# Kernel tuning notes

Hardware: AMD Instinct MI355X
Metric: run time of the kernel (lower is better)

## Reference

```python
import jax, jax.numpy as jnp
import numpy as np

BATCH_SIZE = 4096
DIM = 128
TEMPERATURE = 0.5
EPS = 1e-8


def setup_inputs() -> dict:
    key = jax.random.key(0)
    k1, k2 = jax.random.split(key)
    z_i = jax.random.normal(k1, (BATCH_SIZE, DIM), dtype=jnp.float32)
    z_j = jax.random.normal(k2, (BATCH_SIZE, DIM), dtype=jnp.float32)
    return {"z_i": z_i, "z_j": z_j}


def reference(z_i, z_j):
    B = z_i.shape[0]
    N = 2 * B
    z = jnp.concatenate([z_i, z_j], axis=0)  # [N, D]
    # cosine similarity = matmul of L2-normalized rows (avoids the NxNxD broadcast)
    zn = z / jnp.maximum(jnp.linalg.norm(z, axis=1, keepdims=True), EPS)
    sim = (zn @ zn.T) / TEMPERATURE  # [N, N]
    idx = jnp.arange(N)
    # positive pair: row i pairs with row (i+B) mod N (covers both diag offsets +B and -B)
    pos = sim[idx, (idx + B) % N]  # [N]
    # CE over logits [pos, negatives]; the logit set per row is the full sim row
    # minus the self-similarity (diagonal). Mask diagonal with a large negative.
    neg_inf = jnp.asarray(-1e9, sim.dtype)
    sim_masked = jnp.where(idx[:, None] == idx[None, :], neg_inf, sim)
    lse = jax.nn.logsumexp(sim_masked, axis=1)  # [N]
    # CrossEntropyLoss(reduction='sum') with label 0 (the positive), divided by N
    loss = jnp.sum(lse - pos) / N
    return loss
```

## Files before the change

### kernel.cpp

```cpp
#include <hip/hip_runtime.h>
#include <cstdint>


#define BROWS 4096
#define NROWS 8192
#define ROWB  256
#define CSPL  24
#define CT32  256
#define BRT   256
#define TILEB 8192

typedef __attribute__((ext_vector_type(8))) __bf16    bf16x8;
typedef __attribute__((ext_vector_type(4))) float     f32x4;
typedef __attribute__((ext_vector_type(4))) uint32_t  u32x4;

#define K1F 2.8853900817779268f
#define LN2F 0.69314718055994531f
#define BC8(x) __builtin_bit_cast(bf16x8, x)

__device__ __forceinline__ uint16_t f2bf(float f) {
    uint32_t u = __builtin_bit_cast(uint32_t, f);
    u = (u + 0x7FFFu + ((u >> 16) & 1u)) >> 16;
    return (uint16_t)u;
}
__device__ __forceinline__ float bf2f(uint16_t b) {
    return __builtin_bit_cast(float, ((uint32_t)b) << 16);
}
__device__ __forceinline__ void gload_lds16(const void* g, void* l) {
    __builtin_amdgcn_global_load_lds(
        (const __attribute__((address_space(1))) void*)g,
        (__attribute__((address_space(3))) void*)l, 16, 0, 0);
}

__global__ __launch_bounds__(256) void k_normalize(
    const float* __restrict__ zi, const float* __restrict__ zj,
    uint16_t* __restrict__ znA, uint16_t* __restrict__ znB,
    float* __restrict__ out)
{
    if (blockIdx.x == 0 && threadIdx.x == 0) out[0] = 0.f;

    int tid  = threadIdx.x;
    int lane = tid & 63;
    int wid  = tid >> 6;
    int li   = lane & 7;
    int row  = blockIdx.x * 32 + wid * 8 + (lane >> 3);

    const float* src = (row < BROWS) ? (zi + (size_t)row * 128)
                                     : (zj + (size_t)(row - BROWS) * 128);
    float4 v[4];
    const float4* s4 = (const float4*)(src + li * 16);
#pragma unroll
    for (int c = 0; c < 4; ++c) v[c] = s4[c];

    float ss = 0.f;
#pragma unroll
    for (int c = 0; c < 4; ++c)
        ss += v[c].x*v[c].x + v[c].y*v[c].y + v[c].z*v[c].z + v[c].w*v[c].w;
#pragma unroll
    for (int off = 1; off < 8; off <<= 1) ss += __shfl_xor(ss, off);

    float scale = 1.0f / fmaxf(sqrtf(ss), 1e-8f);

    float e[16];
#pragma unroll
    for (int c = 0; c < 4; ++c) {
        e[c*4+0] = v[c].x * scale; e[c*4+1] = v[c].y * scale;
        e[c*4+2] = v[c].z * scale; e[c*4+3] = v[c].w * scale;
    }
    uint32_t wB[8], wA[8];
#pragma unroll
    for (int q = 0; q < 8; ++q) {
        wB[q] = (uint32_t)f2bf(e[2*q])       | ((uint32_t)f2bf(e[2*q+1])       << 16);
        wA[q] = (uint32_t)f2bf(e[2*q] * K1F) | ((uint32_t)f2bf(e[2*q+1] * K1F) << 16);
    }
    uint4* dB = (uint4*)((char*)znB + (size_t)row * ROWB + li * 32);
    dB[0] = make_uint4(wB[0], wB[1], wB[2], wB[3]);
    dB[1] = make_uint4(wB[4], wB[5], wB[6], wB[7]);
    uint4* dA = (uint4*)((char*)znA + (size_t)row * ROWB + li * 32);
    dA[0] = make_uint4(wA[0], wA[1], wA[2], wA[3]);
    dA[1] = make_uint4(wA[4], wA[5], wA[6], wA[7]);
}

__global__ __launch_bounds__(256)
__attribute__((amdgpu_waves_per_eu(3, 3)))
void k_simlse(
    const uint16_t* __restrict__ znA, const uint16_t* __restrict__ znB,
    float* __restrict__ partial)
{
    __shared__ __align__(16) char lds[3][TILEB];

    const char* zA = (const char*)znA;
    const char* zB = (const char*)znB;
    int tid  = threadIdx.x;
    int lane = tid & 63;
    int wid  = tid >> 6;
    int lo16 = lane & 15;
    int hi4  = lane >> 4;
    int rowBase = blockIdx.x * BRT + wid * 64;

    u32x4 a[4][4];
#pragma unroll
    for (int rt = 0; rt < 4; ++rt) {
        const char* ap = zA + (size_t)(rowBase + rt * 16 + lo16) * ROWB + hi4 * 16;
#pragma unroll
        for (int kf = 0; kf < 4; ++kf)
            a[rt][kf] = *(const u32x4*)(ap + kf * 64);
    }

    float rs[4][4];
#pragma unroll
    for (int rt = 0; rt < 4; ++rt)
#pragma unroll
        for (int r = 0; r < 4; ++r) rs[rt][r] = 0.f;

    int t0 = (CT32 * blockIdx.y) / CSPL;
    int t1 = (CT32 * (blockIdx.y + 1)) / CSPL;
    int nt = t1 - t0;

    const char* gsrc = zB + (size_t)t0 * TILEB
                     + ((tid * 16) ^ (((tid >> 4) & 7) << 4));
    int xorv = (lo16 & 7) << 4;

#define STAGE(sel, t) do {                                                     \
        const char* g_ = gsrc + (size_t)(t) * TILEB;                           \
        gload_lds16(g_,        &lds[sel][wid * 1024]);                         \
        gload_lds16(g_ + 4096, &lds[sel][4096 + wid * 1024]);                  \
    } while (0)

#define COMPUTE(sel) do {                                                        \
        _Pragma("unroll")                                                        \
        for (int ct = 0; ct < 2; ++ct) {                                         \
            const char* lb_ = &lds[sel][ct * 4096 + lo16 * 256];                 \
            u32x4 bf[4];                                                         \
            _Pragma("unroll")                                                    \
            for (int kf = 0; kf < 4; ++kf)                                       \
                bf[kf] = *(const u32x4*)(lb_ + ((hi4 * 16 + kf * 64) ^ xorv));   \
            f32x4 ac0 = {0.f,0.f,0.f,0.f}, ac1 = {0.f,0.f,0.f,0.f};              \
            f32x4 ac2 = {0.f,0.f,0.f,0.f}, ac3 = {0.f,0.f,0.f,0.f};              \
            _Pragma("unroll")                                                    \
            for (int kf = 0; kf < 4; ++kf) {                                     \
                bf16x8 bk_ = BC8(bf[kf]);                                        \
                ac0 = __builtin_amdgcn_mfma_f32_16x16x32_bf16(BC8(a[0][kf]), bk_, ac0, 0, 0, 0); \
                ac1 = __builtin_amdgcn_mfma_f32_16x16x32_bf16(BC8(a[1][kf]), bk_, ac1, 0, 0, 0); \
                ac2 = __builtin_amdgcn_mfma_f32_16x16x32_bf16(BC8(a[2][kf]), bk_, ac2, 0, 0, 0); \
                ac3 = __builtin_amdgcn_mfma_f32_16x16x32_bf16(BC8(a[3][kf]), bk_, ac3, 0, 0, 0); \
            }                                                                    \
            _Pragma("unroll")                                                    \
            for (int r = 0; r < 4; ++r) {                                        \
                rs[0][r] += __builtin_amdgcn_exp2f(ac0[r]);                      \
                rs[1][r] += __builtin_amdgcn_exp2f(ac1[r]);                      \
                rs[2][r] += __builtin_amdgcn_exp2f(ac2[r]);                      \
                rs[3][r] += __builtin_amdgcn_exp2f(ac3[r]);                      \
            }                                                                    \
        }                                                                        \
    } while (0)

    STAGE(0, 0);
    STAGE(1, 1);

    int t = 0;
    for (; t < nt - 1; ++t) {
        asm volatile("s_waitcnt vmcnt(2)" ::: "memory");
        __builtin_amdgcn_s_barrier();
        __builtin_amdgcn_sched_barrier(0);
        COMPUTE(t % 3);
        if (t + 2 < nt) STAGE((t + 2) % 3, t + 2);
    }
    asm volatile("s_waitcnt vmcnt(0)" ::: "memory");
    __builtin_amdgcn_s_barrier();
    __builtin_amdgcn_sched_barrier(0);
    COMPUTE(t % 3);

#undef STAGE
#undef COMPUTE

#pragma unroll
    for (int rt = 0; rt < 4; ++rt)
#pragma unroll
        for (int r = 0; r < 4; ++r) {
            float s = rs[rt][r];
            s += __shfl_xor(s, 1);  s += __shfl_xor(s, 2);
            s += __shfl_xor(s, 4);  s += __shfl_xor(s, 8);
            if (lo16 == 0) {
                int row = rowBase + rt * 16 + hi4 * 4 + r;
                partial[blockIdx.y * NROWS + row] = s;
            }
        }
}

__global__ __launch_bounds__(256) void k_finalize(
    const uint16_t* __restrict__ znA, const uint16_t* __restrict__ znB,
    const float* __restrict__ partial, float* __restrict__ out)
{
    int tid = threadIdx.x;
    int r   = tid >> 3;
    int sub = tid & 7;
    int i = blockIdx.x * 32 + r;

    float S = 0.f;
#pragma unroll
    for (int k = 0; k < 3; ++k) S += partial[(size_t)(sub + k * 8) * NROWS + i];

    int j = (i + BROWS) & (NROWS - 1);
    const uint4* rAi = (const uint4*)((const char*)znA + (size_t)i * ROWB);
    const uint4* rBi = (const uint4*)((const char*)znB + (size_t)i * ROWB);
    const uint4* rBj = (const uint4*)((const char*)znB + (size_t)j * ROWB);
    float adot = 0.f;
    float sdot = 0.f;
#pragma unroll
    for (int cc = 0; cc < 2; ++cc) {
        int c = sub * 2 + cc;
        uint4 ua = rAi[c], ub = rBi[c], vb = rBj[c];
        const uint32_t* pa = (const uint32_t*)&ua;
        const uint32_t* pb = (const uint32_t*)&ub;
        const uint32_t* pv = (const uint32_t*)&vb;
#pragma unroll
        for (int q = 0; q < 4; ++q) {
            float a0 = bf2f((uint16_t)(pa[q] & 0xffffu)), a1 = bf2f((uint16_t)(pa[q] >> 16));
            float b0 = bf2f((uint16_t)(pb[q] & 0xffffu)), b1 = bf2f((uint16_t)(pb[q] >> 16));
            float v0 = bf2f((uint16_t)(pv[q] & 0xffffu)), v1 = bf2f((uint16_t)(pv[q] >> 16));
            adot += a0 * v0 + a1 * v1;
            sdot += a0 * b0 + a1 * b1;
        }
    }
#pragma unroll
    for (int off = 1; off < 8; off <<= 1) {
        S    += __shfl_xor(S, off);
        adot += __shfl_xor(adot, off);
        sdot += __shfl_xor(sdot, off);
    }

    float c = 0.f;
    if (sub == 0) {
        S -= __builtin_amdgcn_exp2f(sdot);
        c = LN2F * (__builtin_amdgcn_logf(S) - adot);
    }
#pragma unroll
    for (int off = 1; off < 64; off <<= 1) c += __shfl_xor(c, off);
    __shared__ float wsum[4];
    int lane = tid & 63, wid = tid >> 6;
    if (lane == 0) wsum[wid] = c;
    __syncthreads();
    if (tid == 0)
        atomicAdd(out, (wsum[0] + wsum[1] + wsum[2] + wsum[3])
                         * (1.0f / (float)NROWS));
}

extern "C" void kernel_launch(void* const* d_in, const int* in_sizes, int n_in,
                              void* d_out, int out_size, void* d_ws, size_t ws_size,
                              hipStream_t stream)
{
    const float* zi = (const float*)d_in[0];
    const float* zj = (const float*)d_in[1];
    float* out = (float*)d_out;

    char* ws = (char*)d_ws;
    uint16_t* znA      = (uint16_t*)ws;
    uint16_t* znB      = (uint16_t*)(ws + (size_t)NROWS * ROWB);
    float*    partial  = (float*)(ws + 2 * (size_t)NROWS * ROWB);

    k_normalize<<<dim3(256), dim3(256), 0, stream>>>(zi, zj, znA, znB, out);
    k_simlse  <<<dim3(32, CSPL), dim3(256), 0, stream>>>(znA, znB, partial);
    k_finalize<<<dim3(256), dim3(256), 0, stream>>>(znA, znB, partial, out);
}
```

Baseline: 35.67 us.

## Software-pipeline exp2 of previous MFMA results with next LDS reads and MFMAs

Restructures the tile loop so the exp2 accumulation of one column subtile overlaps the LDS reads and MFMA issue of the next. It double-buffers the accumulators, adds explicit lgkmcnt fences, raises wave priority around MFMA clusters, and adds an extra barrier per half-tile. The aim is to hide transcendental and LDS latency behind matrix ops. In exchange it uses more registers and an additional barrier, which may reduce occupancy.

```diff
diff --git a/kernel.cpp b/kernel.cpp
--- a/kernel.cpp
+++ b/kernel.cpp
@@ -121,58 +121,114 @@
                      + ((tid * 16) ^ (((tid >> 4) & 7) << 4));
     int xorv = (lo16 & 7) << 4;
 
+    u32x4 bf[4];
+    f32x4 cc0, cc1, cc2, cc3;
+    f32x4 pa0, pa1, pa2, pa3;
+
 #define STAGE(sel, t) do {                                                     \
         const char* g_ = gsrc + (size_t)(t) * TILEB;                           \
         gload_lds16(g_,        &lds[sel][wid * 1024]);                         \
         gload_lds16(g_ + 4096, &lds[sel][4096 + wid * 1024]);                  \
     } while (0)
 
-#define COMPUTE(sel) do {                                                        \
-        _Pragma("unroll")                                                        \
-        for (int ct = 0; ct < 2; ++ct) {                                         \
-            const char* lb_ = &lds[sel][ct * 4096 + lo16 * 256];                 \
-            u32x4 bf[4];                                                         \
-            _Pragma("unroll")                                                    \
-            for (int kf = 0; kf < 4; ++kf)                                       \
-                bf[kf] = *(const u32x4*)(lb_ + ((hi4 * 16 + kf * 64) ^ xorv));   \
-            f32x4 ac0 = {0.f,0.f,0.f,0.f}, ac1 = {0.f,0.f,0.f,0.f};              \
-            f32x4 ac2 = {0.f,0.f,0.f,0.f}, ac3 = {0.f,0.f,0.f,0.f};              \
-            _Pragma("unroll")                                                    \
-            for (int kf = 0; kf < 4; ++kf) {                                     \
-                bf16x8 bk_ = BC8(bf[kf]);                                        \
-                ac0 = __builtin_amdgcn_mfma_f32_16x16x32_bf16(BC8(a[0][kf]), bk_, ac0, 0, 0, 0); \
-                ac1 = __builtin_amdgcn_mfma_f32_16x16x32_bf16(BC8(a[1][kf]), bk_, ac1, 0, 0, 0); \
-                ac2 = __builtin_amdgcn_mfma_f32_16x16x32_bf16(BC8(a[2][kf]), bk_, ac2, 0, 0, 0); \
-                ac3 = __builtin_amdgcn_mfma_f32_16x16x32_bf16(BC8(a[3][kf]), bk_, ac3, 0, 0, 0); \
-            }                                                                    \
-            _Pragma("unroll")                                                    \
-            for (int r = 0; r < 4; ++r) {                                        \
-                rs[0][r] += __builtin_amdgcn_exp2f(ac0[r]);                      \
-                rs[1][r] += __builtin_amdgcn_exp2f(ac1[r]);                      \
-                rs[2][r] += __builtin_amdgcn_exp2f(ac2[r]);                      \
-                rs[3][r] += __builtin_amdgcn_exp2f(ac3[r]);                      \
-            }                                                                    \
-        }                                                                        \
+#define DSREAD(sel, ct) do {                                                   \
+        const char* lb_ = &lds[sel][(ct) * 4096 + lo16 * 256];                 \
+        bf[0] = *(const u32x4*)(lb_ + ((hi4 * 16 +   0) ^ xorv));              \
+        bf[1] = *(const u32x4*)(lb_ + ((hi4 * 16 +  64) ^ xorv));              \
+        bf[2] = *(const u32x4*)(lb_ + ((hi4 * 16 + 128) ^ xorv));              \
+        bf[3] = *(const u32x4*)(lb_ + ((hi4 * 16 + 192) ^ xorv));              \
+    } while (0)
+
+#define MFMASET(D0, D1, D2, D3) do {                                           \
+        D0 = (f32x4){0.f,0.f,0.f,0.f}; D1 = (f32x4){0.f,0.f,0.f,0.f};          \
+        D2 = (f32x4){0.f,0.f,0.f,0.f}; D3 = (f32x4){0.f,0.f,0.f,0.f};          \
+        _Pragma("unroll")                                                      \
+        for (int kf = 0; kf < 4; ++kf) {                                       \
+            bf16x8 bk_ = BC8(bf[kf]);                                          \
+            D0 = __builtin_amdgcn_mfma_f32_16x16x32_bf16(BC8(a[0][kf]), bk_, D0, 0, 0, 0); \
+            D1 = __builtin_amdgcn_mfma_f32_16x16x32_bf16(BC8(a[1][kf]), bk_, D1, 0, 0, 0); \
+            D2 = __builtin_amdgcn_mfma_f32_16x16x32_bf16(BC8(a[2][kf]), bk_, D2, 0, 0, 0); \
+            D3 = __builtin_amdgcn_mfma_f32_16x16x32_bf16(BC8(a[3][kf]), bk_, D3, 0, 0, 0); \
+        }                                                                      \
+    } while (0)
+
+#define EXPSET(P0, P1, P2, P3) do {                                            \
+        _Pragma("unroll")                                                      \
+        for (int r = 0; r < 4; ++r) {                                          \
+            rs[0][r] += __builtin_amdgcn_exp2f(P0[r]);                         \
+            rs[1][r] += __builtin_amdgcn_exp2f(P1[r]);                         \
+            rs[2][r] += __builtin_amdgcn_exp2f(P2[r]);                         \
+            rs[3][r] += __builtin_amdgcn_exp2f(P3[r]);                         \
+        }                                                                      \
+    } while (0)
+
+#define LGKM_FENCE() do {                                                      \
+        asm volatile("s_waitcnt lgkmcnt(0)" ::: "memory");                     \
+        __builtin_amdgcn_sched_barrier(0);                                     \
+    } while (0)
+
+#define MFMA_CLUSTER(D0, D1, D2, D3) do {                                      \
+        __builtin_amdgcn_s_setprio(1);                                         \
+        MFMASET(D0, D1, D2, D3);                                               \
+        __builtin_amdgcn_s_setprio(0);                                         \
     } while (0)
 
     STAGE(0, 0);
     STAGE(1, 1);
 
-    int t = 0;
-    for (; t < nt - 1; ++t) {
+    asm volatile("s_waitcnt vmcnt(2)" ::: "memory");
+    __builtin_amdgcn_s_barrier();
+    __builtin_amdgcn_sched_barrier(0);
+    DSREAD(0, 0);
+    if (2 < nt) STAGE(2, 2);
+    LGKM_FENCE();
+    MFMA_CLUSTER(cc0, cc1, cc2, cc3);
+    __builtin_amdgcn_s_barrier();
+    DSREAD(0, 1);
+    EXPSET(cc0, cc1, cc2, cc3);
+    LGKM_FENCE();
+    MFMA_CLUSTER(pa0, pa1, pa2, pa3);
+
+    for (int t = 1; t < nt - 1; ++t) {
         asm volatile("s_waitcnt vmcnt(2)" ::: "memory");
         __builtin_amdgcn_s_barrier();
         __builtin_amdgcn_sched_barrier(0);
-        COMPUTE(t % 3);
+        int sel = t % 3;
+        DSREAD(sel, 0);
+        EXPSET(pa0, pa1, pa2, pa3);
         if (t + 2 < nt) STAGE((t + 2) % 3, t + 2);
-    }
+        LGKM_FENCE();
+        MFMA_CLUSTER(cc0, cc1, cc2, cc3);
+        __builtin_amdgcn_s_barrier();
+        DSREAD(sel, 1);
+        EXPSET(cc0, cc1, cc2, cc3);
+        LGKM_FENCE();
+        MFMA_CLUSTER(pa0, pa1, pa2, pa3);
+    }
+
     asm volatile("s_waitcnt vmcnt(0)" ::: "memory");
     __builtin_amdgcn_s_barrier();
     __builtin_amdgcn_sched_barrier(0);
-    COMPUTE(t % 3);
+    {
+        int sel = (nt - 1) % 3;
+        DSREAD(sel, 0);
+        EXPSET(pa0, pa1, pa2, pa3);
+        LGKM_FENCE();
+        MFMA_CLUSTER(cc0, cc1, cc2, cc3);
+        __builtin_amdgcn_s_barrier();
+        DSREAD(sel, 1);
+        EXPSET(cc0, cc1, cc2, cc3);
+        LGKM_FENCE();
+        MFMA_CLUSTER(pa0, pa1, pa2, pa3);
+    }
+    EXPSET(pa0, pa1, pa2, pa3);
 
 #undef STAGE
-#undef COMPUTE
+#undef DSREAD
+#undef MFMASET
+#undef EXPSET
+#undef LGKM_FENCE
+#undef MFMA_CLUSTER
 
 #pragma unroll
     for (int rt = 0; rt < 4; ++rt)
```

Result: no change. 36.35 us (+1.9%).
